# Kernel tuning notes

Measured on AMD Instinct MI355X. Metric: run time of the kernel, lower is better.

Reference implementation:

```python
import jax, jax.numpy as jnp
import numpy as np

B, S, F = 4, 2048, 512
H, DK, DV, FILT = 8, 64, 64, 512

def setup_inputs() -> dict:
    key = jax.random.key(0)
    ks = jax.random.split(key, 11)
    sc_in = 1.0 / np.sqrt(F)
    sc_o = 1.0 / np.sqrt(H * DV)
    return {
        "x_q": jax.random.normal(ks[0], (B, S, F), jnp.float32),
        "x_k": jax.random.normal(ks[1], (B, S, F), jnp.float32),
        "x_v": jax.random.normal(ks[2], (B, S, F), jnp.float32),
        "Wq": jax.random.normal(ks[3], (H, F, DK), jnp.float32) * sc_in,
        "bq": jax.random.normal(ks[4], (H, DK), jnp.float32) * 0.01,
        "Wk": jax.random.normal(ks[5], (H, F, DK), jnp.float32) * sc_in,
        "bk": jax.random.normal(ks[6], (H, DK), jnp.float32) * 0.01,
        "Wv": jax.random.normal(ks[7], (H, F, DV), jnp.float32) * sc_in,
        "bv": jax.random.normal(ks[8], (H, DV), jnp.float32) * 0.01,
        "Wo": jax.random.normal(ks[9], (H * DV, FILT), jnp.float32) * sc_o,
        "bo": jax.random.normal(ks[10], (FILT,), jnp.float32) * 0.01,
    }

def reference(x_q, x_k, x_v, Wq, bq, Wk, bk, Wv, bv, Wo, bo):
    d_k = Wq.shape[-1]
    # per-head Dense projections, batched over heads: [B,H,S,dk/dv]
    q = jnp.einsum("bsf,hfk->bhsk", x_q, Wq) + bq[:, None, :]
    k = jnp.einsum("bsf,hfk->bhsk", x_k, Wk) + bk[:, None, :]
    v = jnp.einsum("bsf,hfv->bhsv", x_v, Wv) + bv[:, None, :]
    # scaled dot-product attention (scale by 1/sqrt(d_k) as in map_fn)
    scores = jnp.einsum("bhsk,bhtk->bhst", q, k) / jnp.sqrt(jnp.asarray(d_k, q.dtype))
    attn = jax.nn.softmax(scores, axis=-1)
    out = jnp.einsum("bhst,bhtv->bhsv", attn, v)
    # concat heads along feature dim -> [B,S,H*DV], then output linear
    bsz, h, s, dv = out.shape
    concat = out.transpose(0, 2, 1, 3).reshape(bsz, s, h * dv)
    return concat @ Wo + bo
```

## Files before the change

### kernel.cpp

```cpp
#include <hip/hip_runtime.h>

#define B_    4
#define S_    2048
#define H_    8
#define M_    (B_ * S_)

typedef __bf16    bf16_t;
typedef _Float16  f16_t;
typedef __bf16   bf16x8 __attribute__((ext_vector_type(8)));
typedef __bf16   bf16x4 __attribute__((ext_vector_type(4)));
typedef _Float16 f16x8  __attribute__((ext_vector_type(8)));
typedef float    f32x16 __attribute__((ext_vector_type(16)));

union B8 { uint4 u; bf16x8 v; bf16_t e[8]; };
union B4 { uint2 u; bf16x4 v; bf16_t e[4]; };
union H8 { uint4 u; f16x8  v; f16_t  e[8]; };
union H4 { uint2 u; f16_t  e[4]; };

#define QSCALE 0.1803368801111204f

__global__ __launch_bounds__(256) void convert_w(
    const float* __restrict__ w0, const float* __restrict__ w1,
    const float* __restrict__ w2, bf16_t* __restrict__ t0,
    bf16_t* __restrict__ t1, bf16_t* __restrict__ t2)
{
    __shared__ float T[64][65];
    const float* W  = blockIdx.z == 0 ? w0 : blockIdx.z == 1 ? w1 : w2;
    bf16_t*      Wt = blockIdx.z == 0 ? t0 : blockIdx.z == 1 ? t1 : t2;
    const int h  = blockIdx.y;
    const int k0 = blockIdx.x * 64;
    const int tid = threadIdx.x;
    const int row = tid & 63, q4 = tid >> 6;

    const float* Wh = W + (size_t)h * 512 * 64;
    #pragma unroll
    for (int i = 0; i < 4; ++i) {
        int fq = q4 * 4 + i;
        float4 v = *(const float4*)(Wh + (size_t)(k0 + row) * 64 + fq * 4);
        T[row][fq * 4 + 0] = v.x; T[row][fq * 4 + 1] = v.y;
        T[row][fq * 4 + 2] = v.z; T[row][fq * 4 + 3] = v.w;
    }
    __syncthreads();
    bf16_t* Wth = Wt + (size_t)h * 64 * 512;
    #pragma unroll
    for (int i = 0; i < 4; ++i) {
        int kq = q4 * 4 + i;
        B4 o;
        #pragma unroll
        for (int j = 0; j < 4; ++j) o.e[j] = (bf16_t)T[kq * 4 + j][row];
        *(uint2*)(Wth + (size_t)row * 512 + k0 + kq * 4) = o.u;
    }
}

__global__ __launch_bounds__(256) void convert_wo(
    const float* __restrict__ Wo, f16_t* __restrict__ Wot)
{
    __shared__ float T[64][65];
    const int k0 = blockIdx.x * 64;
    const int n0 = blockIdx.y * 64;
    const int tid = threadIdx.x;
    const int row = tid & 63, q4 = tid >> 6;

    #pragma unroll
    for (int i = 0; i < 4; ++i) {
        int fq = q4 * 4 + i;
        float4 v = *(const float4*)(Wo + (size_t)(k0 + row) * 512 + n0 + fq * 4);
        T[row][fq * 4 + 0] = v.x; T[row][fq * 4 + 1] = v.y;
        T[row][fq * 4 + 2] = v.z; T[row][fq * 4 + 3] = v.w;
    }
    __syncthreads();
    #pragma unroll
    for (int i = 0; i < 4; ++i) {
        int kq = q4 * 4 + i;
        H4 o;
        #pragma unroll
        for (int j = 0; j < 4; ++j) o.e[j] = (f16_t)T[kq * 4 + j][row];
        *(uint2*)(Wot + (size_t)(n0 + row) * 512 + k0 + kq * 4) = o.u;
    }
}

__global__ __launch_bounds__(256) void proj_tiled(
    const float* __restrict__ xq, const float* __restrict__ xk,
    const float* __restrict__ xv,
    const bf16_t* __restrict__ Wtq, const bf16_t* __restrict__ Wtk,
    const bf16_t* __restrict__ Wtv,
    const float* __restrict__ bq, const float* __restrict__ bk,
    const float* __restrict__ bv,
    bf16_t* __restrict__ Qb, bf16_t* __restrict__ Kb, bf16_t* __restrict__ Vt)
{
    __shared__ bf16_t As[128 * 72];
    __shared__ bf16_t Bs[128 * 72];

    const int z = blockIdx.z;
    const float*  X    = z == 0 ? xq  : z == 1 ? xk  : xv;
    const bf16_t* Wt   = z == 0 ? Wtq : z == 1 ? Wtk : Wtv;
    const float*  bias = z == 0 ? bq  : z == 1 ? bk  : bv;

    const int tid  = threadIdx.x;
    const int wave = tid >> 6, lane = tid & 63;
    const int l31  = lane & 31, half = lane >> 5;
    const int m0   = blockIdx.x * 128;
    const int n0   = blockIdx.y * 128;
    const int mw   = (wave & 1) * 64;
    const int nw   = (wave >> 1) * 64;

    const int sr = tid >> 1;
    const int sc = (tid & 1) * 32;

    f32x16 acc[2][2];
    #pragma unroll
    for (int mt = 0; mt < 2; ++mt)
        #pragma unroll
        for (int nt = 0; nt < 2; ++nt)
            #pragma unroll
            for (int i = 0; i < 16; ++i) acc[mt][nt][i] = 0.0f;

    for (int k0 = 0; k0 < 512; k0 += 64) {
        __syncthreads();
        const float*  ap = X  + (size_t)(m0 + sr) * 512 + k0 + sc;
        const bf16_t* bp = Wt + (size_t)(n0 + sr) * 512 + k0 + sc;
        #pragma unroll
        for (int i = 0; i < 4; ++i) {
            float4 fa = *(const float4*)(ap + i * 8);
            float4 fb = *(const float4*)(ap + i * 8 + 4);
            B8 w;
            w.e[0] = (bf16_t)fa.x; w.e[1] = (bf16_t)fa.y;
            w.e[2] = (bf16_t)fa.z; w.e[3] = (bf16_t)fa.w;
            w.e[4] = (bf16_t)fb.x; w.e[5] = (bf16_t)fb.y;
            w.e[6] = (bf16_t)fb.z; w.e[7] = (bf16_t)fb.w;
            *(uint4*)&As[sr * 72 + sc + i * 8] = w.u;
            *(uint4*)&Bs[sr * 72 + sc + i * 8] = *(const uint4*)(bp + i * 8);
        }
        __syncthreads();

        #pragma unroll
        for (int kc = 0; kc < 4; ++kc) {
            B8 a0, a1, b0, b1;
            a0.u = *(const uint4*)&As[(mw + l31)      * 72 + kc * 16 + half * 8];
            a1.u = *(const uint4*)&As[(mw + 32 + l31) * 72 + kc * 16 + half * 8];
            b0.u = *(const uint4*)&Bs[(nw + l31)      * 72 + kc * 16 + half * 8];
            b1.u = *(const uint4*)&Bs[(nw + 32 + l31) * 72 + kc * 16 + half * 8];
            acc[0][0] = __builtin_amdgcn_mfma_f32_32x32x16_bf16(a0.v, b0.v, acc[0][0], 0, 0, 0);
            acc[0][1] = __builtin_amdgcn_mfma_f32_32x32x16_bf16(a0.v, b1.v, acc[0][1], 0, 0, 0);
            acc[1][0] = __builtin_amdgcn_mfma_f32_32x32x16_bf16(a1.v, b0.v, acc[1][0], 0, 0, 0);
            acc[1][1] = __builtin_amdgcn_mfma_f32_32x32x16_bf16(a1.v, b1.v, acc[1][1], 0, 0, 0);
        }
    }

    if (z <= 1) {
        const float sc_ = (z == 0) ? QSCALE : 1.0f;
        bf16_t* Out = (z == 0) ? Qb : Kb;
        #pragma unroll
        for (int mt = 0; mt < 2; ++mt)
            #pragma unroll
            for (int nt = 0; nt < 2; ++nt) {
                int n = n0 + nw + nt * 32 + l31;
                float bv_ = bias[n];
                #pragma unroll
                for (int r = 0; r < 16; ++r) {
                    int m = m0 + mw + mt * 32 + (r & 3) + 8 * (r >> 2) + 4 * half;
                    Out[(size_t)m * 512 + n] = (bf16_t)((acc[mt][nt][r] + bv_) * sc_);
                }
            }
    } else {
        const int b  = m0 >> 11;
        const int sb = (m0 & 2047);
        #pragma unroll
        for (int mt = 0; mt < 2; ++mt)
            #pragma unroll
            for (int nt = 0; nt < 2; ++nt) {
                int n = n0 + nw + nt * 32 + l31;
                float bv_ = bias[n];
                int h = n >> 6, d = n & 63;
                bf16_t* base = Vt + ((size_t)(b * 8 + h) * 64 + d) * 2048 + sb + mw + mt * 32;
                #pragma unroll
                for (int g = 0; g < 4; ++g) {
                    B4 p;
                    #pragma unroll
                    for (int j = 0; j < 4; ++j) p.e[j] = (bf16_t)(acc[mt][nt][g * 4 + j] + bv_);
                    *(uint2*)(base + 8 * g + 4 * half) = p.u;
                }
            }
    }
}

__global__ __launch_bounds__(256) void attn_mfma(
    const bf16_t* __restrict__ Q, const bf16_t* __restrict__ K,
    const bf16_t* __restrict__ Vt, f16_t* __restrict__ O)
{
    __shared__ bf16_t Ks[64 * 72];
    __shared__ bf16_t Vs[64 * 72];

    const int bh  = blockIdx.y;
    const int b   = bh >> 3, h = bh & 7;
    const int q0  = blockIdx.x * 128;
    const int tid = threadIdx.x;
    const int wave = tid >> 6, lane = tid & 63;
    const int l31 = lane & 31, half = lane >> 5;

    bf16x8 qf[4];
    {
        const bf16_t* qp = Q + ((size_t)(b * S_ + q0 + wave * 32 + l31)) * 512 + h * 64 + half * 8;
        #pragma unroll
        for (int ks = 0; ks < 4; ++ks) {
            B8 t; t.u = *(const uint4*)(qp + ks * 16);
            qf[ks] = t.v;
        }
    }

    f32x16 o0, o1;
    #pragma unroll
    for (int i = 0; i < 16; ++i) { o0[i] = 0.0f; o1[i] = 0.0f; }
    float l_i = 0.0f;

    const bf16_t* Kbase = K + ((size_t)b * S_) * 512 + h * 64;
    const bf16_t* Vbase = Vt + ((size_t)bh * 64) * 2048;

    const int kr = tid >> 3, kc8 = tid & 7;
    const int vd = tid >> 2, vj = tid & 3;
    const int kqmap[4] = {0, 2, 1, 3};
    const int vkq = kqmap[vj];

    for (int t0 = 0; t0 < S_; t0 += 64) {
        __syncthreads();
        #pragma unroll
        for (int l = 0; l < 2; ++l) {
            int row = kr + 32 * l;
            *(uint4*)&Ks[row * 72 + kc8 * 8] =
                *(const uint4*)(Kbase + (size_t)(t0 + row) * 512 + kc8 * 8);
        }
        #pragma unroll
        for (int g = 0; g < 4; ++g) {
            *(uint2*)&Vs[vd * 72 + g * 16 + vj * 4] =
                *(const uint2*)(Vbase + (size_t)vd * 2048 + t0 + g * 16 + vkq * 4);
        }
        __syncthreads();

        f32x16 s0, s1;
        #pragma unroll
        for (int i = 0; i < 16; ++i) { s0[i] = 0.0f; s1[i] = 0.0f; }
        #pragma unroll
        for (int ks = 0; ks < 4; ++ks) {
            B8 k0, k1;
            k0.u = *(const uint4*)(&Ks[l31 * 72 + ks * 16 + half * 8]);
            k1.u = *(const uint4*)(&Ks[(32 + l31) * 72 + ks * 16 + half * 8]);
            s0 = __builtin_amdgcn_mfma_f32_32x32x16_bf16(k0.v, qf[ks], s0, 0, 0, 0);
            s1 = __builtin_amdgcn_mfma_f32_32x32x16_bf16(k1.v, qf[ks], s1, 0, 0, 0);
        }

        float ls = 0.0f;
        #pragma unroll
        for (int r = 0; r < 16; ++r) {
            s0[r] = __builtin_amdgcn_exp2f(s0[r]); ls += s0[r];
            s1[r] = __builtin_amdgcn_exp2f(s1[r]); ls += s1[r];
        }
        l_i += ls;

        B8 pf[4];
        #pragma unroll
        for (int j = 0; j < 8; ++j) {
            pf[0].e[j] = (bf16_t)s0[j];
            pf[1].e[j] = (bf16_t)s0[8 + j];
            pf[2].e[j] = (bf16_t)s1[j];
            pf[3].e[j] = (bf16_t)s1[8 + j];
        }

        #pragma unroll
        for (int c = 0; c < 4; ++c) {
            B8 va, vb;
            va.u = *(const uint4*)(&Vs[l31 * 72 + c * 16 + half * 8]);
            vb.u = *(const uint4*)(&Vs[(32 + l31) * 72 + c * 16 + half * 8]);
            o0 = __builtin_amdgcn_mfma_f32_32x32x16_bf16(va.v, pf[c].v, o0, 0, 0, 0);
            o1 = __builtin_amdgcn_mfma_f32_32x32x16_bf16(vb.v, pf[c].v, o1, 0, 0, 0);
        }
    }

    l_i += __shfl_xor(l_i, 32);
    float inv = 1.0f / l_i;
    f16_t* Ob = O + ((size_t)(b * S_ + q0 + wave * 32 + l31)) * 512 + h * 64;
    #pragma unroll
    for (int g = 0; g < 4; ++g) {
        H4 a, c;
        #pragma unroll
        for (int j = 0; j < 4; ++j) {
            a.e[j] = (f16_t)(o0[g * 4 + j] * inv);
            c.e[j] = (f16_t)(o1[g * 4 + j] * inv);
        }
        int d = 8 * g + 4 * half;
        *(uint2*)(Ob + d)      = a.u;
        *(uint2*)(Ob + 32 + d) = c.u;
    }
}

__global__ __launch_bounds__(256) void gemm_out_tiled(
    const f16_t* __restrict__ A, const f16_t* __restrict__ Wot,
    const float* __restrict__ bias, float* __restrict__ C)
{
    __shared__ f16_t As[64 * 72];
    __shared__ f16_t Bs[64 * 72];

    const int tid  = threadIdx.x;
    const int wave = tid >> 6, lane = tid & 63;
    const int l31  = lane & 31, half = lane >> 5;
    const int m0   = blockIdx.x * 64;
    const int n0   = blockIdx.y * 64;
    const int mw   = (wave & 1) * 32;
    const int nw   = (wave >> 1) * 32;

    const int sr  = tid >> 2;
    const int so  = (tid & 3) * 16;

    f32x16 acc;
    #pragma unroll
    for (int i = 0; i < 16; ++i) acc[i] = 0.0f;

    for (int k0 = 0; k0 < 512; k0 += 64) {
        __syncthreads();
        const f16_t* ap = A   + (size_t)(m0 + sr) * 512 + k0 + so;
        const f16_t* bp = Wot + (size_t)(n0 + sr) * 512 + k0 + so;
        *(uint4*)&As[sr * 72 + so]     = *(const uint4*)(ap);
        *(uint4*)&As[sr * 72 + so + 8] = *(const uint4*)(ap + 8);
        *(uint4*)&Bs[sr * 72 + so]     = *(const uint4*)(bp);
        *(uint4*)&Bs[sr * 72 + so + 8] = *(const uint4*)(bp + 8);
        __syncthreads();

        #pragma unroll
        for (int kc = 0; kc < 4; ++kc) {
            H8 a, b;
            a.u = *(const uint4*)&As[(mw + l31) * 72 + kc * 16 + half * 8];
            b.u = *(const uint4*)&Bs[(nw + l31) * 72 + kc * 16 + half * 8];
            acc = __builtin_amdgcn_mfma_f32_32x32x16_f16(a.v, b.v, acc, 0, 0, 0);
        }
    }

    const int n = n0 + nw + l31;
    const float bias0 = bias[n];
    #pragma unroll
    for (int r = 0; r < 16; ++r) {
        int m = m0 + mw + (r & 3) + 8 * (r >> 2) + 4 * half;
        C[(size_t)m * 512 + n] = acc[r] + bias0;
    }
}

extern "C" void kernel_launch(void* const* d_in, const int* in_sizes, int n_in,
                              void* d_out, int out_size, void* d_ws, size_t ws_size,
                              hipStream_t stream)
{
    const float* x_q = (const float*)d_in[0];
    const float* x_k = (const float*)d_in[1];
    const float* x_v = (const float*)d_in[2];
    const float* Wq  = (const float*)d_in[3];
    const float* bq  = (const float*)d_in[4];
    const float* Wk  = (const float*)d_in[5];
    const float* bk  = (const float*)d_in[6];
    const float* Wv  = (const float*)d_in[7];
    const float* bv  = (const float*)d_in[8];
    const float* Wo  = (const float*)d_in[9];
    const float* bo  = (const float*)d_in[10];
    float* out = (float*)d_out;

    char* W = (char*)d_ws;
    bf16_t* Wtq = (bf16_t*)W;
    bf16_t* Wtk = Wtq + (size_t)8 * 64 * 512;
    bf16_t* Wtv = Wtk + (size_t)8 * 64 * 512;
    f16_t*  Wot = (f16_t*)(Wtv + (size_t)8 * 64 * 512);
    bf16_t* Qb  = (bf16_t*)(Wot + (size_t)512 * 512);
    bf16_t* Kb  = Qb + (size_t)M_ * 512;
    bf16_t* Vt  = Kb + (size_t)M_ * 512;
    f16_t*  AO  = (f16_t*)(Vt + (size_t)M_ * 512);

    convert_w<<<dim3(8, 8, 3), 256, 0, stream>>>(Wq, Wk, Wv, Wtq, Wtk, Wtv);
    convert_wo<<<dim3(8, 8), 256, 0, stream>>>(Wo, Wot);

    proj_tiled<<<dim3(64, 4, 3), 256, 0, stream>>>(
        x_q, x_k, x_v, Wtq, Wtk, Wtv, bq, bk, bv, Qb, Kb, Vt);

    attn_mfma<<<dim3(S_ / 128, B_ * H_), 256, 0, stream>>>(Qb, Kb, Vt, AO);

    gemm_out_tiled<<<dim3(128, 8), 256, 0, stream>>>(AO, Wot, bo, out);
}
```

Before: 226.0 us.

## Split attention KV range across two wave groups and prefetch GEMM tiles into registers

The attention kernel now launches 512 threads per block. Two groups of four waves each process half of the key sequence for the same query tile, and their partial outputs and sums are merged through shared memory at the end. This doubles the waves available to hide latency, since the grid had only 512 blocks. The projection and output GEMMs gain register prefetch of the next K tile, so global loads overlap the MFMA loop. In exchange, register pressure and shared memory use grow, and the combine step adds an extra synchronisation.

```diff
diff --git a/kernel.cpp b/kernel.cpp
--- a/kernel.cpp
+++ b/kernel.cpp
@@ -107,6 +107,19 @@
     const int sr = tid >> 1;
     const int sc = (tid & 1) * 32;
 
+    float4 ra0[4], ra1[4];
+    uint4  rb[4];
+    {
+        const float*  ap = X  + (size_t)(m0 + sr) * 512 + sc;
+        const bf16_t* bp = Wt + (size_t)(n0 + sr) * 512 + sc;
+        #pragma unroll
+        for (int i = 0; i < 4; ++i) {
+            ra0[i] = *(const float4*)(ap + i * 8);
+            ra1[i] = *(const float4*)(ap + i * 8 + 4);
+            rb[i]  = *(const uint4*)(bp + i * 8);
+        }
+    }
+
     f32x16 acc[2][2];
     #pragma unroll
     for (int mt = 0; mt < 2; ++mt)
@@ -117,19 +130,25 @@
 
     for (int k0 = 0; k0 < 512; k0 += 64) {
         __syncthreads();
-        const float*  ap = X  + (size_t)(m0 + sr) * 512 + k0 + sc;
-        const bf16_t* bp = Wt + (size_t)(n0 + sr) * 512 + k0 + sc;
         #pragma unroll
         for (int i = 0; i < 4; ++i) {
-            float4 fa = *(const float4*)(ap + i * 8);
-            float4 fb = *(const float4*)(ap + i * 8 + 4);
             B8 w;
-            w.e[0] = (bf16_t)fa.x; w.e[1] = (bf16_t)fa.y;
-            w.e[2] = (bf16_t)fa.z; w.e[3] = (bf16_t)fa.w;
-            w.e[4] = (bf16_t)fb.x; w.e[5] = (bf16_t)fb.y;
-            w.e[6] = (bf16_t)fb.z; w.e[7] = (bf16_t)fb.w;
+            w.e[0] = (bf16_t)ra0[i].x; w.e[1] = (bf16_t)ra0[i].y;
+            w.e[2] = (bf16_t)ra0[i].z; w.e[3] = (bf16_t)ra0[i].w;
+            w.e[4] = (bf16_t)ra1[i].x; w.e[5] = (bf16_t)ra1[i].y;
+            w.e[6] = (bf16_t)ra1[i].z; w.e[7] = (bf16_t)ra1[i].w;
             *(uint4*)&As[sr * 72 + sc + i * 8] = w.u;
-            *(uint4*)&Bs[sr * 72 + sc + i * 8] = *(const uint4*)(bp + i * 8);
+            *(uint4*)&Bs[sr * 72 + sc + i * 8] = rb[i];
+        }
+        if (k0 + 64 < 512) {
+            const float*  ap = X  + (size_t)(m0 + sr) * 512 + k0 + 64 + sc;
+            const bf16_t* bp = Wt + (size_t)(n0 + sr) * 512 + k0 + 64 + sc;
+            #pragma unroll
+            for (int i = 0; i < 4; ++i) {
+                ra0[i] = *(const float4*)(ap + i * 8);
+                ra1[i] = *(const float4*)(ap + i * 8 + 4);
+                rb[i]  = *(const uint4*)(bp + i * 8);
+            }
         }
         __syncthreads();
 
@@ -184,12 +203,13 @@
     }
 }
 
-__global__ __launch_bounds__(256) void attn_mfma(
+__global__ __launch_bounds__(512) void attn_mfma(
     const bf16_t* __restrict__ Q, const bf16_t* __restrict__ K,
     const bf16_t* __restrict__ Vt, f16_t* __restrict__ O)
 {
-    __shared__ bf16_t Ks[64 * 72];
-    __shared__ bf16_t Vs[64 * 72];
+    __shared__ char smraw[36864];
+    bf16_t* KsBuf = (bf16_t*)smraw;
+    bf16_t* VsBuf = KsBuf + 2 * 64 * 72;
 
     const int bh  = blockIdx.y;
     const int b   = bh >> 3, h = bh & 7;
@@ -197,10 +217,11 @@
     const int tid = threadIdx.x;
     const int wave = tid >> 6, lane = tid & 63;
     const int l31 = lane & 31, half = lane >> 5;
+    const int qsub = wave & 3, ksplit = wave >> 2;
 
     bf16x8 qf[4];
     {
-        const bf16_t* qp = Q + ((size_t)(b * S_ + q0 + wave * 32 + l31)) * 512 + h * 64 + half * 8;
+        const bf16_t* qp = Q + ((size_t)(b * S_ + q0 + qsub * 32 + l31)) * 512 + h * 64 + half * 8;
         #pragma unroll
         for (int ks = 0; ks < 4; ++ks) {
             B8 t; t.u = *(const uint4*)(qp + ks * 16);
@@ -216,23 +237,30 @@
     const bf16_t* Kbase = K + ((size_t)b * S_) * 512 + h * 64;
     const bf16_t* Vbase = Vt + ((size_t)bh * 64) * 2048;
 
-    const int kr = tid >> 3, kc8 = tid & 7;
-    const int vd = tid >> 2, vj = tid & 3;
+    const int sbuf = tid >> 8;
+    const int p    = tid & 255;
+    const int kr = p >> 3, kc8 = p & 7;
+    const int vd = p >> 2, vj = p & 3;
     const int kqmap[4] = {0, 2, 1, 3};
     const int vkq = kqmap[vj];
-
-    for (int t0 = 0; t0 < S_; t0 += 64) {
+    bf16_t* KsS = KsBuf + sbuf * (64 * 72);
+    bf16_t* VsS = VsBuf + sbuf * (64 * 72);
+    const bf16_t* KsC = KsBuf + ksplit * (64 * 72);
+    const bf16_t* VsC = VsBuf + ksplit * (64 * 72);
+
+    for (int t0 = 0; t0 < 1024; t0 += 64) {
+        const int tb = sbuf * 1024 + t0;
         __syncthreads();
         #pragma unroll
         for (int l = 0; l < 2; ++l) {
             int row = kr + 32 * l;
-            *(uint4*)&Ks[row * 72 + kc8 * 8] =
-                *(const uint4*)(Kbase + (size_t)(t0 + row) * 512 + kc8 * 8);
+            *(uint4*)&KsS[row * 72 + kc8 * 8] =
+                *(const uint4*)(Kbase + (size_t)(tb + row) * 512 + kc8 * 8);
         }
         #pragma unroll
         for (int g = 0; g < 4; ++g) {
-            *(uint2*)&Vs[vd * 72 + g * 16 + vj * 4] =
-                *(const uint2*)(Vbase + (size_t)vd * 2048 + t0 + g * 16 + vkq * 4);
+            *(uint2*)&VsS[vd * 72 + g * 16 + vj * 4] =
+                *(const uint2*)(Vbase + (size_t)vd * 2048 + tb + g * 16 + vkq * 4);
         }
         __syncthreads();
 
@@ -242,8 +270,8 @@
         #pragma unroll
         for (int ks = 0; ks < 4; ++ks) {
             B8 k0, k1;
-            k0.u = *(const uint4*)(&Ks[l31 * 72 + ks * 16 + half * 8]);
-            k1.u = *(const uint4*)(&Ks[(32 + l31) * 72 + ks * 16 + half * 8]);
+            k0.u = *(const uint4*)(&KsC[l31 * 72 + ks * 16 + half * 8]);
+            k1.u = *(const uint4*)(&KsC[(32 + l31) * 72 + ks * 16 + half * 8]);
             s0 = __builtin_amdgcn_mfma_f32_32x32x16_bf16(k0.v, qf[ks], s0, 0, 0, 0);
             s1 = __builtin_amdgcn_mfma_f32_32x32x16_bf16(k1.v, qf[ks], s1, 0, 0, 0);
         }
@@ -268,27 +296,44 @@
         #pragma unroll
         for (int c = 0; c < 4; ++c) {
             B8 va, vb;
-            va.u = *(const uint4*)(&Vs[l31 * 72 + c * 16 + half * 8]);
-            vb.u = *(const uint4*)(&Vs[(32 + l31) * 72 + c * 16 + half * 8]);
+            va.u = *(const uint4*)(&VsC[l31 * 72 + c * 16 + half * 8]);
+            vb.u = *(const uint4*)(&VsC[(32 + l31) * 72 + c * 16 + half * 8]);
             o0 = __builtin_amdgcn_mfma_f32_32x32x16_bf16(va.v, pf[c].v, o0, 0, 0, 0);
             o1 = __builtin_amdgcn_mfma_f32_32x32x16_bf16(vb.v, pf[c].v, o1, 0, 0, 0);
         }
     }
 
     l_i += __shfl_xor(l_i, 32);
-    float inv = 1.0f / l_i;
-    f16_t* Ob = O + ((size_t)(b * S_ + q0 + wave * 32 + l31)) * 512 + h * 64;
-    #pragma unroll
-    for (int g = 0; g < 4; ++g) {
-        H4 a, c;
-        #pragma unroll
-        for (int j = 0; j < 4; ++j) {
-            a.e[j] = (f16_t)(o0[g * 4 + j] * inv);
-            c.e[j] = (f16_t)(o1[g * 4 + j] * inv);
-        }
-        int d = 8 * g + 4 * half;
-        *(uint2*)(Ob + d)      = a.u;
-        *(uint2*)(Ob + 32 + d) = c.u;
+    __syncthreads();
+    float* co = (float*)smraw;
+    float* cl = co + 4 * 32 * 68;
+    if (ksplit == 1) {
+        float* reg = co + qsub * (32 * 68);
+        #pragma unroll
+        for (int r = 0; r < 16; ++r) {
+            reg[r * 68 + lane]        = o0[r];
+            reg[(16 + r) * 68 + lane] = o1[r];
+        }
+        cl[qsub * 64 + lane] = l_i;
+    }
+    __syncthreads();
+    if (ksplit == 0) {
+        float* reg = co + qsub * (32 * 68);
+        float inv = 1.0f / (l_i + cl[qsub * 64 + lane]);
+        f16_t* Ob = O + ((size_t)(b * S_ + q0 + qsub * 32 + l31)) * 512 + h * 64;
+        #pragma unroll
+        for (int g = 0; g < 4; ++g) {
+            H4 a, c;
+            #pragma unroll
+            for (int j = 0; j < 4; ++j) {
+                int r = g * 4 + j;
+                a.e[j] = (f16_t)((o0[r] + reg[r * 68 + lane]) * inv);
+                c.e[j] = (f16_t)((o1[r] + reg[(16 + r) * 68 + lane]) * inv);
+            }
+            int d = 8 * g + 4 * half;
+            *(uint2*)(Ob + d)      = a.u;
+            *(uint2*)(Ob + 32 + d) = c.u;
+        }
     }
 }
 
@@ -310,18 +355,30 @@
     const int sr  = tid >> 2;
     const int so  = (tid & 3) * 16;
 
+    uint4 pA0, pA1, pB0, pB1;
+    {
+        const f16_t* ap = A   + (size_t)(m0 + sr) * 512 + so;
+        const f16_t* bp = Wot + (size_t)(n0 + sr) * 512 + so;
+        pA0 = *(const uint4*)(ap); pA1 = *(const uint4*)(ap + 8);
+        pB0 = *(const uint4*)(bp); pB1 = *(const uint4*)(bp + 8);
+    }
+
     f32x16 acc;
     #pragma unroll
     for (int i = 0; i < 16; ++i) acc[i] = 0.0f;
 
     for (int k0 = 0; k0 < 512; k0 += 64) {
         __syncthreads();
-        const f16_t* ap = A   + (size_t)(m0 + sr) * 512 + k0 + so;
-        const f16_t* bp = Wot + (size_t)(n0 + sr) * 512 + k0 + so;
-        *(uint4*)&As[sr * 72 + so]     = *(const uint4*)(ap);
-        *(uint4*)&As[sr * 72 + so + 8] = *(const uint4*)(ap + 8);
-        *(uint4*)&Bs[sr * 72 + so]     = *(const uint4*)(bp);
-        *(uint4*)&Bs[sr * 72 + so + 8] = *(const uint4*)(bp + 8);
+        *(uint4*)&As[sr * 72 + so]     = pA0;
+        *(uint4*)&As[sr * 72 + so + 8] = pA1;
+        *(uint4*)&Bs[sr * 72 + so]     = pB0;
+        *(uint4*)&Bs[sr * 72 + so + 8] = pB1;
+        if (k0 + 64 < 512) {
+            const f16_t* ap = A   + (size_t)(m0 + sr) * 512 + k0 + 64 + so;
+            const f16_t* bp = Wot + (size_t)(n0 + sr) * 512 + k0 + 64 + so;
+            pA0 = *(const uint4*)(ap); pA1 = *(const uint4*)(ap + 8);
+            pB0 = *(const uint4*)(bp); pB1 = *(const uint4*)(bp + 8);
+        }
         __syncthreads();
 
         #pragma unroll
@@ -375,7 +432,7 @@
     proj_tiled<<<dim3(64, 4, 3), 256, 0, stream>>>(
         x_q, x_k, x_v, Wtq, Wtk, Wtv, bq, bk, bv, Qb, Kb, Vt);
 
-    attn_mfma<<<dim3(S_ / 128, B_ * H_), 256, 0, stream>>>(Qb, Kb, Vt, AO);
+    attn_mfma<<<dim3(S_ / 128, B_ * H_), 512, 0, stream>>>(Qb, Kb, Vt, AO);
 
     gemm_out_tiled<<<dim3(128, 8), 256, 0, stream>>>(AO, Wot, bo, out);
 }
```

Measured after the change: 222.5 us. No clear change (-1.6%).
